# Performance work log

Hardware: AMD Instinct MI355X
Metric: run time of the kernel (lower is better)

The kernel has to match this reference:

```python
import jax, jax.numpy as jnp
import numpy as np

# Dimensions: B=batch, T=decode len, S=source len, E=emb, H=rnn hidden, ENC=encoder size, V=vocab
B, T, S, E, H, ENC, V = 32, 64, 128, 256, 512, 512, 32000


def setup_inputs() -> dict:
    key = jax.random.key(0)
    ks = jax.random.split(key, 12)
    sc = lambda k, shape, s: jax.random.normal(k, shape, jnp.float32) * s
    return {
        "gold_tokens": jax.random.randint(ks[0], (B, T), 0, V),
        "enc_outputs": jax.random.normal(ks[1], (B, S, ENC), jnp.float32),
        "enc_lengths": jax.random.randint(ks[2], (B,), S // 2, S + 1),
        "h0": jnp.zeros((B, H), jnp.float32),
        "c0": jnp.zeros((B, H), jnp.float32),
        # learned parameters
        "embed_table": sc(ks[3], (V, E), 0.02),
        "W_ih": sc(ks[4], (4 * H, E), 0.05),   # torch LSTM gate order: i, f, g, o
        "W_hh": sc(ks[5], (4 * H, H), 0.05),
        "b_ih": jnp.zeros((4 * H,), jnp.float32),
        "b_hh": jnp.zeros((4 * H,), jnp.float32),
        "Wa": sc(ks[6], (H, ENC), 0.05),        # 'general' attention: score = q^T Wa k
        "Wc_w": sc(ks[7], (H, H + ENC), 0.05),  # Wc: Linear(rnn+enc -> ho=rnn)
        "Wc_b": jnp.zeros((H,), jnp.float32),
        "Wo_w": sc(ks[8], (V, H), 0.02),        # Wo: Linear(ho -> vocab)
        "Wo_b": jnp.zeros((V,), jnp.float32),
    }


def reference(gold_tokens, enc_outputs, enc_lengths, h0, c0, embed_table,
              W_ih, W_hh, b_ih, b_hh, Wa, Wc_w, Wc_b, Wo_w, Wo_b):
    S = enc_outputs.shape[1]
    # length mask for attention over encoder states
    mask = jnp.arange(S)[None, :] < enc_lengths[:, None]          # [B, S]
    # precompute Wa @ enc (invariant across decode steps)
    proj_enc = jnp.einsum('he,bse->bsh', Wa, enc_outputs)         # [B, S, H]
    embs = embed_table[gold_tokens]                               # [B, T, E] teacher forcing

    def step(carry, e_t):
        h, c = carry                                              # [B, H] each
        gates = e_t @ W_ih.T + b_ih + h @ W_hh.T + b_hh           # [B, 4H]
        i, f, g, o = jnp.split(gates, 4, axis=-1)
        c = jax.nn.sigmoid(f) * c + jax.nn.sigmoid(i) * jnp.tanh(g)
        h = jax.nn.sigmoid(o) * jnp.tanh(c)
        # general attention: score[b,s] = h[b] . (Wa enc[b,s])
        scores = jnp.einsum('bh,bsh->bs', h, proj_enc)
        scores = jnp.where(mask, scores, jnp.float32(-1e9))
        att = jax.nn.softmax(scores, axis=-1)                     # [B, S]
        ctx = jnp.einsum('bs,bse->be', att, enc_outputs)          # [B, ENC]
        ho = jnp.concatenate([h, ctx], axis=-1) @ Wc_w.T + Wc_b   # [B, H]
        logit = ho @ Wo_w.T + Wo_b                                # [B, V]
        return (h, c), logit

    (_, _), logits = jax.lax.scan(step, (h0, c0), jnp.swapaxes(embs, 0, 1))
    return jnp.swapaxes(logits, 0, 1)                             # [B, T, V]
```

## Files before the change

kernel.cpp:

```cpp
#include <hip/hip_runtime.h>

typedef unsigned short u16;
typedef unsigned int   u32;
typedef __attribute__((ext_vector_type(8))) __bf16 bf16x8;
typedef __attribute__((ext_vector_type(4))) float  f32x4;

#define B_   32
#define T_   64
#define S_   128
#define E_   256
#define H_   512
#define ENC_ 512
#define V_   32000

__device__ __forceinline__ float b2f(u16 u) {
  union { u32 i; float f; } v; v.i = ((u32)u) << 16; return v.f;
}
__device__ __forceinline__ u16 f2b(float f) {
  union { float f; u32 i; } v; v.f = f;
  u32 r = (v.i + 0x7fffu + ((v.i >> 16) & 1u)) >> 16;
  return (u16)r;
}
__device__ __forceinline__ float sigm(float x) { return 1.f / (1.f + __expf(-x)); }

__device__ __forceinline__ void async_ld16(const void* g, void* l) {
  __builtin_amdgcn_global_load_lds((const __attribute__((address_space(1))) u32*)g,
                                   (__attribute__((address_space(3))) u32*)l,
                                   16, 0, 0);
}

__global__ __launch_bounds__(256) void k_cvt(const float* __restrict__ src,
                                             u16* __restrict__ dst, int n4) {
  int i = blockIdx.x * 256 + threadIdx.x;
  if (i < n4) {
    float4 v = ((const float4*)src)[i];
    ushort4 o;
    o.x = f2b(v.x); o.y = f2b(v.y); o.z = f2b(v.z); o.w = f2b(v.w);
    ((ushort4*)dst)[i] = o;
  }
}

template <typename OUT_T>
__global__ __launch_bounds__(256) void gemm_bt(
    const u16* __restrict__ A, int lda,
    const u16* __restrict__ B, int ldb,
    OUT_T* __restrict__ C, int ldc, int K,
    const float* __restrict__ bias1, const float* __restrict__ bias2) {
  __shared__ __align__(16) u16 As[128 * 64];
  __shared__ __align__(16) u16 Bs[128 * 64];

  const int tid  = threadIdx.x;
  int f = blockIdx.y * gridDim.x + blockIdx.x;
  const int nwg = gridDim.x * gridDim.y;
  int g = (nwg & 7) ? f : ((f & 7) * (nwg >> 3) + (f >> 3));
  const int m0 = (g % gridDim.x) * 128;
  const int n0 = (g / gridDim.x) * 128;
  const int wave = tid >> 6, lane = tid & 63;
  const int mw = (wave >> 1) * 64, nw = (wave & 1) * 64;
  const int lr = lane & 15, lq = lane >> 4;

  f32x4 acc[4][4];
#pragma unroll
  for (int i = 0; i < 4; ++i)
#pragma unroll
    for (int j = 0; j < 4; ++j) acc[i][j] = (f32x4){0.f, 0.f, 0.f, 0.f};

  for (int k0 = 0; k0 < K; k0 += 64) {
#pragma unroll
    for (int it = 0; it < 4; ++it) {
      int chunk = it * 256 + tid;
      int row = chunk >> 3;
      int kc  = (chunk & 7) << 3;
      async_ld16(&A[(size_t)(m0 + row) * lda + k0 + kc], &As[chunk << 3]);
    }
#pragma unroll
    for (int it = 0; it < 4; ++it) {
      int chunk = it * 256 + tid;
      int row = chunk >> 3;
      int kc  = (chunk & 7) << 3;
      async_ld16(&B[(size_t)(n0 + row) * ldb + k0 + kc], &Bs[chunk << 3]);
    }
    __syncthreads();
#pragma unroll
    for (int kk = 0; kk < 2; ++kk) {
      bf16x8 af[4], bf[4];
#pragma unroll
      for (int i = 0; i < 4; ++i)
        af[i] = *(const bf16x8*)&As[(mw + i * 16 + lr) * 64 + kk * 32 + lq * 8];
#pragma unroll
      for (int j = 0; j < 4; ++j)
        bf[j] = *(const bf16x8*)&Bs[(nw + j * 16 + lr) * 64 + kk * 32 + lq * 8];
#pragma unroll
      for (int i = 0; i < 4; ++i)
#pragma unroll
        for (int j = 0; j < 4; ++j)
          acc[i][j] = __builtin_amdgcn_mfma_f32_16x16x32_bf16(af[i], bf[j], acc[i][j], 0, 0, 0);
    }
    __syncthreads();
  }

#pragma unroll
  for (int j = 0; j < 4; ++j) {
    int n = n0 + nw + j * 16 + lr;
    float bs = 0.f;
    if (bias1) bs += bias1[n];
    if (bias2) bs += bias2[n];
#pragma unroll
    for (int i = 0; i < 4; ++i) {
#pragma unroll
      for (int r = 0; r < 4; ++r) {
        int m = m0 + mw + i * 16 + lq * 4 + r;
        float v = acc[i][j][r] + bs;
        if constexpr (sizeof(OUT_T) == 2)
          C[(size_t)m * ldc + n] = (OUT_T)f2b(v);
        else
          C[(size_t)m * ldc + n] = v;
      }
    }
  }
}

__global__ __launch_bounds__(256) void k_embed(const int* __restrict__ toks,
                                               const float* __restrict__ table,
                                               u16* __restrict__ emb) {
  int id  = blockIdx.x * 256 + threadIdx.x;
  int row = id >> 6;
  int c4  = (id & 63) << 2;
  int tok = toks[row];
  float4 v = *(const float4*)&table[(size_t)tok * E_ + c4];
  ushort4 o;
  o.x = f2b(v.x); o.y = f2b(v.y); o.z = f2b(v.z); o.w = f2b(v.w);
  *(ushort4*)&emb[(size_t)row * E_ + c4] = o;
}

__global__ __launch_bounds__(256) void k_transpose(const float* __restrict__ Wa,
                                                   u16* __restrict__ WaT) {
  __shared__ float tle[32][33];
  int bx = blockIdx.x * 32;
  int by = blockIdx.y * 32;
  int tid = threadIdx.x;
  for (int i = tid; i < 1024; i += 256) {
    int r = i >> 5, c = i & 31;
    tle[r][c] = Wa[(size_t)(bx + r) * ENC_ + by + c];
  }
  __syncthreads();
  for (int i = tid; i < 1024; i += 256) {
    int r = i >> 5, c = i & 31;
    WaT[(size_t)(by + r) * H_ + bx + c] = f2b(tle[c][r]);
  }
}

__global__ __launch_bounds__(256) void k_lstm(
    const u16* __restrict__ Whh,
    const float* __restrict__ gp,
    const float* __restrict__ c0,
    u16* __restrict__ Hbuf,
    u16* __restrict__ hc) {
  const int blk  = blockIdx.x;
  const int tid  = threadIdx.x;
  const int wave = tid >> 6, lane = tid & 63;
  const int mi = wave >> 1, ni = wave & 1;
  const int lr = lane & 15, lq = lane >> 4;

  const int p    = ni * 16 + lr;
  const int grow = (p >> 3) * H_ + blk * 8 + (p & 7);
  bf16x8 bfr[16];
#pragma unroll
  for (int ks = 0; ks < 16; ++ks)
    bfr[ks] = *(const bf16x8*)&Whh[(size_t)grow * H_ + ks * 32 + lq * 8];

  const int pb = tid >> 3, pj = tid & 7;
  const int hidx = blk * 8 + pj;
  float c = c0[pb * H_ + hidx];

  __shared__ __align__(16) u16 Hs[32 * 512];
  __shared__ float G[32][33];

  const int am = mi * 16 + lr;
  const char* HsA = (const char*)Hs + am * 1024 + ((lq * 16) ^ ((am & 3) << 4));

  float gpr[4];
#pragma unroll
  for (int r = 0; r < 4; ++r)
    gpr[r] = gp[(size_t)((mi * 16 + lq * 4 + r) * T_ + 0) * 2048 + grow];

#pragma unroll
  for (int it = 0; it < 8; ++it) {
    int chunk = it * 256 + tid;
    int src_byte = (chunk * 16) ^ (((chunk >> 6) & 3) << 4);
    async_ld16((const char*)Hbuf + src_byte, &Hs[chunk * 8]);
  }
  __syncthreads();

  for (int t = 0; t < T_; ++t) {
    f32x4 acc = (f32x4){0.f, 0.f, 0.f, 0.f};
#pragma unroll
    for (int ks = 0; ks < 16; ++ks) {
      bf16x8 a = *(const bf16x8*)(HsA + ks * 64);
      acc = __builtin_amdgcn_mfma_f32_16x16x32_bf16(a, bfr[ks], acc, 0, 0, 0);
    }
#pragma unroll
    for (int r = 0; r < 4; ++r)
      G[mi * 16 + lq * 4 + r][p] = acc[r] + gpr[r];
    __syncthreads();

    if (t < T_ - 1) {
#pragma unroll
      for (int r = 0; r < 4; ++r)
        gpr[r] = gp[(size_t)((mi * 16 + lq * 4 + r) * T_ + t + 1) * 2048 + grow];
    }

    float gi = G[pb][pj], gf = G[pb][8 + pj], gg = G[pb][16 + pj], go = G[pb][24 + pj];
    c = sigm(gf) * c + sigm(gi) * tanhf(gg);
    float h = sigm(go) * tanhf(c);
    u16 hb = f2b(h);
    u32 other = (u32)__shfl_xor((int)(u32)hb, 1);
    if (!(tid & 1)) {
      u32 pk = (u32)hb | (other << 16);
      __hip_atomic_store((u32*)&Hbuf[(size_t)(t + 1) * (B_ * H_) + pb * H_ + hidx], pk,
                         __ATOMIC_RELAXED, __HIP_MEMORY_SCOPE_AGENT);
      *(u32*)&hc[(size_t)(pb * T_ + t) * 1024 + hidx] = pk;
    }

    if (t < T_ - 1) {
      const u32* hsrc = (const u32*)&Hbuf[(size_t)(t + 1) * (B_ * H_)];
      u32 tmp[32];
#pragma unroll
      for (int it = 0; it < 32; ++it)
        tmp[it] = __hip_atomic_load(&hsrc[it * 256 + tid], __ATOMIC_RELAXED,
                                    __HIP_MEMORY_SCOPE_AGENT);
      for (;;) {
        u32 bad = 0;
#pragma unroll
        for (int it = 0; it < 32; ++it) bad |= (tmp[it] == 0xFFFFFFFFu);
        if (!bad) break;
#pragma unroll
        for (int it = 0; it < 32; ++it)
          if (tmp[it] == 0xFFFFFFFFu)
            tmp[it] = __hip_atomic_load(&hsrc[it * 256 + tid], __ATOMIC_RELAXED,
                                        __HIP_MEMORY_SCOPE_AGENT);
      }
#pragma unroll
      for (int it = 0; it < 32; ++it) {
        int d  = it * 256 + tid;
        int sw = d ^ ((it & 3) << 2);
        *(u32*)&Hs[(size_t)sw * 2] = tmp[it];
      }
      __syncthreads();
    }
  }
}

__global__ __launch_bounds__(256) void k_attn(
    const u16* __restrict__ q,
    const u16* __restrict__ enc,
    const int* __restrict__ lens,
    u16* __restrict__ hc) {
  const int bt = blockIdx.x;
  const int b  = bt >> 6;
  const int tid = threadIdx.x;
  const int len = lens[b];

  __shared__ float qs[512];
  __shared__ float sc[128];
  __shared__ float red2[256];
  __shared__ float sred[2];

  for (int i = tid; i < 512; i += 256) qs[i] = b2f(q[(size_t)bt * 512 + i]);
  __syncthreads();

  {
    int s = tid & 127, half = tid >> 7;
    const u16* er = &enc[((size_t)b * S_ + s) * 512 + half * 256];
    const float* qb = &qs[half * 256];
    float a = 0.f;
#pragma unroll 4
    for (int k = 0; k < 256; k += 8) {
      uint4 raw = *(const uint4*)&er[k];
      u32 w0 = raw.x, w1 = raw.y, w2 = raw.z, w3 = raw.w;
      union { u32 i; float f; } lo, hi;
      lo.i = w0 << 16;          a += lo.f * qb[k + 0];
      hi.i = w0 & 0xffff0000u;  a += hi.f * qb[k + 1];
      lo.i = w1 << 16;          a += lo.f * qb[k + 2];
      hi.i = w1 & 0xffff0000u;  a += hi.f * qb[k + 3];
      lo.i = w2 << 16;          a += lo.f * qb[k + 4];
      hi.i = w2 & 0xffff0000u;  a += hi.f * qb[k + 5];
      lo.i = w3 << 16;          a += lo.f * qb[k + 6];
      hi.i = w3 & 0xffff0000u;  a += hi.f * qb[k + 7];
    }
    red2[tid] = a;
  }
  __syncthreads();
  if (tid < 128) {
    float v = red2[tid] + red2[tid + 128];
    sc[tid] = (tid < len) ? v : -1e30f;
  }
  __syncthreads();
  if (tid < 64) {
    float m = fmaxf(sc[tid], sc[tid + 64]);
#pragma unroll
    for (int o = 32; o > 0; o >>= 1) m = fmaxf(m, __shfl_down(m, o));
    if (tid == 0) sred[0] = m;
  }
  __syncthreads();
  float mx = sred[0];
  if (tid < 128) sc[tid] = __expf(sc[tid] - mx);
  __syncthreads();
  if (tid < 64) {
    float s2 = sc[tid] + sc[tid + 64];
#pragma unroll
    for (int o = 32; o > 0; o >>= 1) s2 += __shfl_down(s2, o);
    if (tid == 0) sred[1] = s2;
  }
  __syncthreads();
  float inv = 1.0f / sred[1];

  float a0 = 0.f, a1 = 0.f;
  for (int s = 0; s < S_; ++s) {
    float at = sc[s];
    const u16* er = &enc[((size_t)b * S_ + s) * 512];
    a0 += at * b2f(er[tid]);
    a1 += at * b2f(er[tid + 256]);
  }
  hc[(size_t)bt * 1024 + 512 + tid]       = f2b(a0 * inv);
  hc[(size_t)bt * 1024 + 512 + tid + 256] = f2b(a1 * inv);
}

extern "C" void kernel_launch(void* const* d_in, const int* in_sizes, int n_in,
                              void* d_out, int out_size, void* d_ws, size_t ws_size,
                              hipStream_t stream) {
  const int*   toks  = (const int*)d_in[0];
  const float* enc   = (const float*)d_in[1];
  const int*   lens  = (const int*)d_in[2];
  const float* h0    = (const float*)d_in[3];
  const float* c0    = (const float*)d_in[4];
  const float* table = (const float*)d_in[5];
  const float* W_ih  = (const float*)d_in[6];
  const float* W_hh  = (const float*)d_in[7];
  const float* b_ih  = (const float*)d_in[8];
  const float* b_hh  = (const float*)d_in[9];
  const float* Wa    = (const float*)d_in[10];
  const float* Wc_w  = (const float*)d_in[11];
  const float* Wc_b  = (const float*)d_in[12];
  const float* Wo_w  = (const float*)d_in[13];
  const float* Wo_b  = (const float*)d_in[14];
  float* out = (float*)d_out;

  char* ws = (char*)d_ws;
  size_t off = 0;
  auto alloc = [&](size_t bytes) {
    void* pp = ws + off;
    off += (bytes + 255) & ~(size_t)255;
    return pp;
  };
  float* gp    = (float*)alloc((size_t)B_ * T_ * 2048 * 4);
  u16*   emb   = (u16*)alloc((size_t)B_ * T_ * E_ * 2);
  u16*   Hbuf  = (u16*)alloc((size_t)(T_ + 1) * B_ * H_ * 2);
  u16*   hc    = (u16*)alloc((size_t)B_ * T_ * 1024 * 2);
  u16*   q     = (u16*)alloc((size_t)B_ * T_ * ENC_ * 2);
  u16*   WaT   = (u16*)alloc((size_t)ENC_ * H_ * 2);
  u16*   ho    = (u16*)alloc((size_t)B_ * T_ * H_ * 2);
  u16*   Wihb  = (u16*)alloc((size_t)2048 * E_ * 2);
  u16*   Whhb  = (u16*)alloc((size_t)2048 * H_ * 2);
  u16*   Wcwb  = (u16*)alloc((size_t)H_ * 1024 * 2);
  u16*   Wowb  = (u16*)alloc((size_t)V_ * H_ * 2);
  u16*   encb  = (u16*)alloc((size_t)B_ * S_ * ENC_ * 2);
  (void)in_sizes; (void)n_in; (void)out_size; (void)ws_size;

  hipMemsetAsync(Hbuf + (size_t)B_ * H_, 0xFF, (size_t)T_ * B_ * H_ * 2, stream);

  k_cvt<<<(2048 * E_ / 4 + 255) / 256, 256, 0, stream>>>(W_ih, Wihb, 2048 * E_ / 4);
  k_cvt<<<(2048 * H_ / 4 + 255) / 256, 256, 0, stream>>>(W_hh, Whhb, 2048 * H_ / 4);
  k_cvt<<<(H_ * 1024 / 4 + 255) / 256, 256, 0, stream>>>(Wc_w, Wcwb, H_ * 1024 / 4);
  k_cvt<<<(V_ * H_ / 4 + 255) / 256, 256, 0, stream>>>(Wo_w, Wowb, V_ * H_ / 4);
  k_cvt<<<(B_ * S_ * ENC_ / 4 + 255) / 256, 256, 0, stream>>>(enc, encb, B_ * S_ * ENC_ / 4);
  k_cvt<<<(B_ * H_ / 4 + 255) / 256, 256, 0, stream>>>(h0, Hbuf, B_ * H_ / 4);
  k_embed<<<512, 256, 0, stream>>>(toks, table, emb);
  gemm_bt<float><<<dim3(16, 16), 256, 0, stream>>>(emb, E_, Wihb, E_, gp, 2048, E_, b_ih, b_hh);
  k_transpose<<<dim3(16, 16), 256, 0, stream>>>(Wa, WaT);
  k_lstm<<<64, 256, 0, stream>>>(Whhb, gp, c0, Hbuf, hc);
  gemm_bt<u16><<<dim3(16, 4), 256, 0, stream>>>(hc, 1024, WaT, H_, q, ENC_, H_, nullptr, nullptr);
  k_attn<<<B_ * T_, 256, 0, stream>>>(q, encb, lens, hc);
  gemm_bt<u16><<<dim3(16, 4), 256, 0, stream>>>(hc, 1024, Wcwb, 1024, ho, H_, 1024, Wc_b, nullptr);
  gemm_bt<float><<<dim3(16, 250), 256, 0, stream>>>(ho, H_, Wowb, H_, out, V_, H_, Wo_b, nullptr);
}
```

Measured before the change: 867.7 us.

## Load LSTM hidden state directly into registers and use 64x64 tiles for small GEMMs

```diff
diff --git a/kernel.cpp b/kernel.cpp
--- a/kernel.cpp
+++ b/kernel.cpp
@@ -2,6 +2,7 @@
 
 typedef unsigned short u16;
 typedef unsigned int   u32;
+typedef unsigned long long u64;
 typedef __attribute__((ext_vector_type(8))) __bf16 bf16x8;
 typedef __attribute__((ext_vector_type(4))) float  f32x4;
 
@@ -107,6 +108,86 @@
     if (bias2) bs += bias2[n];
 #pragma unroll
     for (int i = 0; i < 4; ++i) {
+#pragma unroll
+      for (int r = 0; r < 4; ++r) {
+        int m = m0 + mw + i * 16 + lq * 4 + r;
+        float v = acc[i][j][r] + bs;
+        if constexpr (sizeof(OUT_T) == 2)
+          C[(size_t)m * ldc + n] = (OUT_T)f2b(v);
+        else
+          C[(size_t)m * ldc + n] = v;
+      }
+    }
+  }
+}
+
+template <typename OUT_T>
+__global__ __launch_bounds__(256) void gemm64(
+    const u16* __restrict__ A, int lda,
+    const u16* __restrict__ B, int ldb,
+    OUT_T* __restrict__ C, int ldc, int K,
+    const float* __restrict__ bias1, const float* __restrict__ bias2) {
+  __shared__ __align__(16) u16 As[64 * 64];
+  __shared__ __align__(16) u16 Bs[64 * 64];
+
+  const int tid  = threadIdx.x;
+  int f = blockIdx.y * gridDim.x + blockIdx.x;
+  const int nwg = gridDim.x * gridDim.y;
+  int g = (nwg & 7) ? f : ((f & 7) * (nwg >> 3) + (f >> 3));
+  const int m0 = (g % gridDim.x) * 64;
+  const int n0 = (g / gridDim.x) * 64;
+  const int wave = tid >> 6, lane = tid & 63;
+  const int mw = (wave >> 1) * 32, nw = (wave & 1) * 32;
+  const int lr = lane & 15, lq = lane >> 4;
+
+  f32x4 acc[2][2];
+#pragma unroll
+  for (int i = 0; i < 2; ++i)
+#pragma unroll
+    for (int j = 0; j < 2; ++j) acc[i][j] = (f32x4){0.f, 0.f, 0.f, 0.f};
+
+  for (int k0 = 0; k0 < K; k0 += 64) {
+#pragma unroll
+    for (int it = 0; it < 2; ++it) {
+      int chunk = it * 256 + tid;
+      int row = chunk >> 3;
+      int kc  = (chunk & 7) << 3;
+      async_ld16(&A[(size_t)(m0 + row) * lda + k0 + kc], &As[chunk << 3]);
+    }
+#pragma unroll
+    for (int it = 0; it < 2; ++it) {
+      int chunk = it * 256 + tid;
+      int row = chunk >> 3;
+      int kc  = (chunk & 7) << 3;
+      async_ld16(&B[(size_t)(n0 + row) * ldb + k0 + kc], &Bs[chunk << 3]);
+    }
+    __syncthreads();
+#pragma unroll
+    for (int kk = 0; kk < 2; ++kk) {
+      bf16x8 af[2], bf[2];
+#pragma unroll
+      for (int i = 0; i < 2; ++i)
+        af[i] = *(const bf16x8*)&As[(mw + i * 16 + lr) * 64 + kk * 32 + lq * 8];
+#pragma unroll
+      for (int j = 0; j < 2; ++j)
+        bf[j] = *(const bf16x8*)&Bs[(nw + j * 16 + lr) * 64 + kk * 32 + lq * 8];
+#pragma unroll
+      for (int i = 0; i < 2; ++i)
+#pragma unroll
+        for (int j = 0; j < 2; ++j)
+          acc[i][j] = __builtin_amdgcn_mfma_f32_16x16x32_bf16(af[i], bf[j], acc[i][j], 0, 0, 0);
+    }
+    __syncthreads();
+  }
+
+#pragma unroll
+  for (int j = 0; j < 2; ++j) {
+    int n = n0 + nw + j * 16 + lr;
+    float bs = 0.f;
+    if (bias1) bs += bias1[n];
+    if (bias2) bs += bias2[n];
+#pragma unroll
+    for (int i = 0; i < 2; ++i) {
 #pragma unroll
       for (int r = 0; r < 4; ++r) {
         int m = m0 + mw + i * 16 + lq * 4 + r;
@@ -173,32 +254,34 @@
   const int hidx = blk * 8 + pj;
   float c = c0[pb * H_ + hidx];
 
-  __shared__ __align__(16) u16 Hs[32 * 512];
   __shared__ float G[32][33];
 
   const int am = mi * 16 + lr;
-  const char* HsA = (const char*)Hs + am * 1024 + ((lq * 16) ^ ((am & 3) << 4));
+
+  u64 af8[32];
+  {
+    const u64* a0p = (const u64*)((const char*)Hbuf + (size_t)am * 1024 + lq * 16);
+#pragma unroll
+    for (int ks = 0; ks < 16; ++ks) {
+      af8[2 * ks]     = a0p[ks * 8];
+      af8[2 * ks + 1] = a0p[ks * 8 + 1];
+    }
+  }
 
   float gpr[4];
 #pragma unroll
   for (int r = 0; r < 4; ++r)
     gpr[r] = gp[(size_t)((mi * 16 + lq * 4 + r) * T_ + 0) * 2048 + grow];
 
-#pragma unroll
-  for (int it = 0; it < 8; ++it) {
-    int chunk = it * 256 + tid;
-    int src_byte = (chunk * 16) ^ (((chunk >> 6) & 3) << 4);
-    async_ld16((const char*)Hbuf + src_byte, &Hs[chunk * 8]);
-  }
-  __syncthreads();
-
   for (int t = 0; t < T_; ++t) {
     f32x4 acc = (f32x4){0.f, 0.f, 0.f, 0.f};
 #pragma unroll
     for (int ks = 0; ks < 16; ++ks) {
-      bf16x8 a = *(const bf16x8*)(HsA + ks * 64);
-      acc = __builtin_amdgcn_mfma_f32_16x16x32_bf16(a, bfr[ks], acc, 0, 0, 0);
-    }
+      union { u64 q[2]; bf16x8 v; } uu;
+      uu.q[0] = af8[2 * ks]; uu.q[1] = af8[2 * ks + 1];
+      acc = __builtin_amdgcn_mfma_f32_16x16x32_bf16(uu.v, bfr[ks], acc, 0, 0, 0);
+    }
+    __syncthreads();
 #pragma unroll
     for (int r = 0; r < 4; ++r)
       G[mi * 16 + lq * 4 + r][p] = acc[r] + gpr[r];
@@ -223,30 +306,28 @@
     }
 
     if (t < T_ - 1) {
-      const u32* hsrc = (const u32*)&Hbuf[(size_t)(t + 1) * (B_ * H_)];
-      u32 tmp[32];
-#pragma unroll
-      for (int it = 0; it < 32; ++it)
-        tmp[it] = __hip_atomic_load(&hsrc[it * 256 + tid], __ATOMIC_RELAXED,
-                                    __HIP_MEMORY_SCOPE_AGENT);
+      __builtin_amdgcn_s_sleep(12);
+      const u64* hsrc = (const u64*)((const char*)Hbuf +
+          ((size_t)(t + 1) * (B_ * H_) + (size_t)am * H_) * 2 + lq * 16);
+#pragma unroll
+      for (int ks = 0; ks < 16; ++ks) {
+        af8[2 * ks] = __hip_atomic_load(&hsrc[ks * 8], __ATOMIC_RELAXED,
+                                        __HIP_MEMORY_SCOPE_AGENT);
+        af8[2 * ks + 1] = __hip_atomic_load(&hsrc[ks * 8 + 1], __ATOMIC_RELAXED,
+                                            __HIP_MEMORY_SCOPE_AGENT);
+      }
       for (;;) {
         u32 bad = 0;
 #pragma unroll
-        for (int it = 0; it < 32; ++it) bad |= (tmp[it] == 0xFFFFFFFFu);
+        for (int i = 0; i < 32; ++i) bad |= (af8[i] == ~0ull);
         if (!bad) break;
-#pragma unroll
-        for (int it = 0; it < 32; ++it)
-          if (tmp[it] == 0xFFFFFFFFu)
-            tmp[it] = __hip_atomic_load(&hsrc[it * 256 + tid], __ATOMIC_RELAXED,
-                                        __HIP_MEMORY_SCOPE_AGENT);
+        __builtin_amdgcn_s_sleep(2);
+#pragma unroll
+        for (int i = 0; i < 32; ++i)
+          if (af8[i] == ~0ull)
+            af8[i] = __hip_atomic_load(&hsrc[(i >> 1) * 8 + (i & 1)],
+                                       __ATOMIC_RELAXED, __HIP_MEMORY_SCOPE_AGENT);
       }
-#pragma unroll
-      for (int it = 0; it < 32; ++it) {
-        int d  = it * 256 + tid;
-        int sw = d ^ ((it & 3) << 2);
-        *(u32*)&Hs[(size_t)sw * 2] = tmp[it];
-      }
-      __syncthreads();
     }
   }
 }
@@ -379,8 +460,8 @@
   gemm_bt<float><<<dim3(16, 16), 256, 0, stream>>>(emb, E_, Wihb, E_, gp, 2048, E_, b_ih, b_hh);
   k_transpose<<<dim3(16, 16), 256, 0, stream>>>(Wa, WaT);
   k_lstm<<<64, 256, 0, stream>>>(Whhb, gp, c0, Hbuf, hc);
-  gemm_bt<u16><<<dim3(16, 4), 256, 0, stream>>>(hc, 1024, WaT, H_, q, ENC_, H_, nullptr, nullptr);
+  gemm64<u16><<<dim3(32, 8), 256, 0, stream>>>(hc, 1024, WaT, H_, q, ENC_, H_, nullptr, nullptr);
   k_attn<<<B_ * T_, 256, 0, stream>>>(q, encb, lens, hc);
-  gemm_bt<u16><<<dim3(16, 4), 256, 0, stream>>>(hc, 1024, Wcwb, 1024, ho, H_, 1024, Wc_b, nullptr);
+  gemm64<u16><<<dim3(32, 8), 256, 0, stream>>>(hc, 1024, Wcwb, 1024, ho, H_, 1024, Wc_b, nullptr);
   gemm_bt<float><<<dim3(16, 250), 256, 0, stream>>>(ho, H_, Wowb, H_, out, V_, H_, Wo_b, nullptr);
 }
```

New measurement: 944.4 us. +8.8%, slower.
